# Kernel optimization log

Hardware: AMD Instinct MI355X
Metric: run time of the kernel (lower is better)

## Reference

```python
import jax, jax.numpy as jnp
import numpy as np

N_NODES = 100000


def gcn_conv(x, edge_index, W, b):
    """PyG-style GCNConv: h = D^-1/2 (A+I) D^-1/2 (x W) + b."""
    n = x.shape[0]
    loop = jnp.arange(n)
    src = jnp.concatenate([edge_index[0], loop])  # [E+N]
    dst = jnp.concatenate([edge_index[1], loop])  # [E+N]
    # degree computed on destination nodes (PyG gcn_norm with self-loops)
    deg = jnp.zeros((n,), x.dtype).at[dst].add(1.0)
    dinv = jnp.where(deg > 0, jax.lax.rsqrt(deg), 0.0)
    norm = dinv[src] * dinv[dst]  # [E+N]
    h = x @ W  # [n, out]
    msg = h[src] * norm[:, None]  # gather + scale
    out = jax.ops.segment_sum(msg, dst, num_segments=n)  # scatter-add
    return out + b


def setup_inputs() -> dict:
    key = jax.random.key(0)
    ks = jax.random.split(key, 8)
    F_in, H, C = 64, 64, 32
    x = jax.random.normal(ks[0], (N_NODES, F_in), dtype=jnp.float32)
    edge_index = jax.random.randint(ks[1], (2, 1200000), 0, N_NODES, dtype=jnp.int64)
    W1 = jax.random.normal(ks[2], (F_in, H), dtype=jnp.float32) / np.sqrt(F_in)
    b1 = jnp.zeros((H,), jnp.float32)
    W2 = jax.random.normal(ks[3], (H, H), dtype=jnp.float32) / np.sqrt(H)
    b2 = jnp.zeros((H,), jnp.float32)
    Wc = jax.random.normal(ks[4], (H, C), dtype=jnp.float32) / np.sqrt(H)
    bc = jnp.zeros((C,), jnp.float32)
    return {"x": x, "edge_index": edge_index, "W1": W1, "b1": b1,
            "W2": W2, "b2": b2, "Wc": Wc, "bc": bc}


def reference(x, edge_index, W1, b1, W2, b2, Wc, bc):
    h = jnp.tanh(gcn_conv(x, edge_index, W1, b1))
    h = jnp.tanh(gcn_conv(h, edge_index, W2, b2))
    out = h @ Wc + bc
    return (out, h)
```

## Files before the change

kernel.cpp:

```cpp
#include <hip/hip_runtime.h>
#include <hip/hip_bf16.h>
#include <stdint.h>

#define CB_SHIFT 11
#define CB_NODES 2048
#define CAP 28672
#define PT 4096

static __device__ inline uint16_t f2bf(float f) {
    union { float f; uint32_t u; } v; v.f = f;
    uint32_t r = v.u + 0x7FFFu + ((v.u >> 16) & 1u);
    return (uint16_t)(r >> 16);
}
static __device__ inline float bflo(uint32_t u) {
    union { uint32_t u; float f; } v; v.u = u << 16; return v.f;
}
static __device__ inline float bfhi(uint32_t u) {
    union { uint32_t u; float f; } v; v.u = u & 0xFFFF0000u; return v.f;
}
static __device__ inline float tanh_fast(float x) {
    x = fminf(fmaxf(x, -20.f), 20.f);
    float e = __expf(2.f * x);
    return fmaf(-2.f, __builtin_amdgcn_rcpf(e + 1.f), 1.f);
}

__global__ __launch_bounds__(256) void k_init(const uint32_t* __restrict__ e, int E,
                                              int* __restrict__ flag, int* __restrict__ gcur) {
    int t = threadIdx.x;
    if (t < 64) {
        gcur[t] = 0;
        int cnt = E < 1024 ? E : 1024;
        int nz = 0;
        for (int i = t; i < cnt; i += 64) nz |= (e[2 * i + 1] != 0u);
        int any = __any(nz);
        if (t == 0) *flag = any ? 0 : 1;
    }
}

__global__ __launch_bounds__(256) void k_part(const uint32_t* __restrict__ e, int E,
                                              const int* __restrict__ flag,
                                              int* __restrict__ gcur,
                                              uint32_t* __restrict__ parts) {
    __shared__ int sh_hist[64], sh_off[64], sh_base[64];
    __shared__ uint32_t sh_buf[PT];
    __shared__ uint16_t sh_bkt[PT];
    int t = threadIdx.x;
    int tile0 = blockIdx.x * PT;
    int is64 = *flag;
    if (t < 64) sh_hist[t] = 0;
    __syncthreads();

    uint32_t rec[16]; int cb[16], rank[16];
    const uint2* e2p = (const uint2*)e;
    for (int j = 0; j < 16; ++j) {
        int idx = tile0 + j * 256 + t;
        cb[j] = -1;
        if (idx < E) {
            uint32_t s, d;
            if (is64) { s = e2p[idx].x; d = e2p[E + idx].x; }
            else      { s = e[idx];     d = e[E + idx]; }
            rec[j] = (s << CB_SHIFT) | (d & (CB_NODES - 1));
            cb[j] = (int)(d >> CB_SHIFT);
            rank[j] = atomicAdd(&sh_hist[cb[j]], 1);
        }
    }
    __syncthreads();
    if (t < 64) {
        int cnt = sh_hist[t];
        int incl = cnt;
        for (int o = 1; o < 64; o <<= 1) {
            int v = __shfl_up(incl, o);
            if (t >= o) incl += v;
        }
        sh_off[t] = incl - cnt;
        sh_base[t] = (cnt > 0) ? atomicAdd(&gcur[t], cnt) : 0;
    }
    __syncthreads();
    for (int j = 0; j < 16; ++j) {
        if (cb[j] >= 0) {
            int slot = sh_off[cb[j]] + rank[j];
            sh_buf[slot] = rec[j];
            sh_bkt[slot] = (uint16_t)cb[j];
        }
    }
    __syncthreads();
    int total = min(PT, E - tile0);
    for (int i = t; i < total; i += 256) {
        int b = sh_bkt[i];
        int dest = sh_base[b] + (i - sh_off[b]);
        parts[(size_t)b * CAP + dest] = sh_buf[i];
    }
}

__global__ __launch_bounds__(1024) void k_build(const uint32_t* __restrict__ parts,
                                                const int* __restrict__ gcur,
                                                float* __restrict__ dinv,
                                                int* __restrict__ rowbeg,
                                                int* __restrict__ rowend,
                                                uint32_t* __restrict__ col, int N) {
    __shared__ int hist[CB_NODES], cur[CB_NODES], wsum[16];
    int t = threadIdx.x, cb = blockIdx.x;
    int lane = t & 63, w = t >> 6;
    for (int i = t; i < CB_NODES; i += 1024) hist[i] = 0;
    __syncthreads();
    int cnt = gcur[cb];
    const uint32_t* rp = parts + (size_t)cb * CAP;
    for (int i = t; i < cnt; i += 1024) atomicAdd(&hist[rp[i] & (CB_NODES - 1)], 1);
    __syncthreads();
    int h0 = hist[2 * t], h1 = hist[2 * t + 1];
    int s = h0 + h1;
    int incl = s;
    for (int o = 1; o < 64; o <<= 1) {
        int v = __shfl_up(incl, o);
        if (lane >= o) incl += v;
    }
    if (lane == 63) wsum[w] = incl;
    __syncthreads();
    if (t < 16) {
        int v = wsum[t];
        int inc2 = v;
        for (int o = 1; o < 16; o <<= 1) {
            int u = __shfl_up(inc2, o);
            if (t >= o) inc2 += u;
        }
        wsum[t] = inc2 - v;
    }
    __syncthreads();
    int ex = wsum[w] + incl - s;
    int b0 = ex, b1 = ex + h0;
    cur[2 * t] = b0;
    cur[2 * t + 1] = b1;
    int n0 = cb * CB_NODES;
    int base = cb * CAP;
    if (n0 + 2 * t < N) {
        rowbeg[n0 + 2 * t] = base + b0;
        rowend[n0 + 2 * t] = base + b0 + h0;
        dinv[n0 + 2 * t] = rsqrtf((float)(h0 + 1));
    }
    if (n0 + 2 * t + 1 < N) {
        rowbeg[n0 + 2 * t + 1] = base + b1;
        rowend[n0 + 2 * t + 1] = base + b1 + h1;
        dinv[n0 + 2 * t + 1] = rsqrtf((float)(h1 + 1));
    }
    __syncthreads();
    for (int i = t; i < cnt; i += 1024) {
        uint32_t rec = rp[i];
        int pos = atomicAdd(&cur[rec & (CB_NODES - 1)], 1);
        col[base + pos] = rec >> CB_SHIFT;
    }
}

__global__ __launch_bounds__(256) void k_gemm(const float* __restrict__ A,
                                              const float* __restrict__ W,
                                              const float* __restrict__ dinv,
                                              uint16_t* __restrict__ out, int N) {
    __shared__ __align__(16) float xT[64 * 68];
    __shared__ __align__(16) float Wl[64 * 64];
    int t = threadIdx.x;
#pragma unroll
    for (int j = 0; j < 16; ++j) Wl[j * 256 + t] = W[j * 256 + t];
    int n0 = blockIdx.x * 64;
    int nvalid = min(64, N - n0);
#pragma unroll
    for (int j = 0; j < 4; ++j) {
        int flat = j * 256 + t;
        int node = flat >> 4;
        int k4 = (flat & 15) * 4;
        float4 v = make_float4(0.f, 0.f, 0.f, 0.f);
        if (node < nvalid) v = *(const float4*)&A[(size_t)(n0 + node) * 64 + k4];
        xT[(k4 + 0) * 68 + node] = v.x;
        xT[(k4 + 1) * 68 + node] = v.y;
        xT[(k4 + 2) * 68 + node] = v.z;
        xT[(k4 + 3) * 68 + node] = v.w;
    }
    __syncthreads();
    int ng = t >> 4, cg = t & 15;
    float acc[4][4] = {};
#pragma unroll 8
    for (int k = 0; k < 64; ++k) {
        float4 a = *(const float4*)&xT[k * 68 + 4 * ng];
        float4 b = *(const float4*)&Wl[k * 64 + 4 * cg];
        float av[4] = {a.x, a.y, a.z, a.w};
        float bv[4] = {b.x, b.y, b.z, b.w};
#pragma unroll
        for (int i = 0; i < 4; ++i)
#pragma unroll
            for (int j = 0; j < 4; ++j) acc[i][j] = fmaf(av[i], bv[j], acc[i][j]);
    }
#pragma unroll
    for (int i = 0; i < 4; ++i) {
        int ln = 4 * ng + i;
        if (ln < nvalid) {
            int n = n0 + ln;
            float dv = dinv[n];
            ushort4 o;
            o.x = f2bf(acc[i][0] * dv);
            o.y = f2bf(acc[i][1] * dv);
            o.z = f2bf(acc[i][2] * dv);
            o.w = f2bf(acc[i][3] * dv);
            *(ushort4*)&out[(size_t)n * 64 + 4 * cg] = o;
        }
    }
}

__global__ __launch_bounds__(512) void k_agg(const uint16_t* __restrict__ h,
                                             const int* __restrict__ rowbeg,
                                             const int* __restrict__ rowend,
                                             const uint32_t* __restrict__ col,
                                             const float* __restrict__ dinv,
                                             const float* __restrict__ bias,
                                             const float* __restrict__ ,
                                             float* __restrict__ out, int N) {
    int t = threadIdx.x;
    int lane = t & 63, wid = t >> 6;
    int slot = lane >> 3;
    int g = lane & 7;
    const uint4* hp = (const uint4*)h;
    float bv[8];
#pragma unroll
    for (int j = 0; j < 8; ++j) bv[j] = bias[g * 8 + j];
    int n = (blockIdx.x * 8 + wid) * 8 + slot;
    int rs = 0, deg = 0;
    if (n < N) { rs = rowbeg[n]; deg = rowend[n] - rs; }
    int m = deg;
#pragma unroll
    for (int o = 1; o < 64; o <<= 1) m = max(m, __shfl_xor(m, o));
    float acc[8] = {};
#pragma unroll 2
    for (int it = 0; it < m; ++it) {
        if (it < deg) {
            int src = (int)col[rs + it];
            uint4 v = hp[(size_t)src * 8 + g];
            acc[0] += bflo(v.x); acc[1] += bfhi(v.x);
            acc[2] += bflo(v.y); acc[3] += bfhi(v.y);
            acc[4] += bflo(v.z); acc[5] += bfhi(v.z);
            acc[6] += bflo(v.w); acc[7] += bfhi(v.w);
        }
    }
    if (n < N) {
        float di = dinv[n];
        uint4 v = hp[(size_t)n * 8 + g];
        float hn[8] = {bflo(v.x), bfhi(v.x), bflo(v.y), bfhi(v.y),
                       bflo(v.z), bfhi(v.z), bflo(v.w), bfhi(v.w)};
        __align__(16) float o[8];
#pragma unroll
        for (int j = 0; j < 8; ++j)
            o[j] = tanh_fast(di * (acc[j] + hn[j]) + bv[j]);
        *(float4*)&out[(size_t)n * 64 + g * 8]     = *(float4*)&o[0];
        *(float4*)&out[(size_t)n * 64 + g * 8 + 4] = *(float4*)&o[4];
    }
}

__global__ __launch_bounds__(256) void k_cls(const float* __restrict__ A,
                                             const float* __restrict__ W,
                                             const float* __restrict__ bc,
                                             float* __restrict__ out, int N) {
    __shared__ __align__(16) float xT[64 * 68];
    __shared__ __align__(16) float Wl[64 * 32];
    int t = threadIdx.x;
#pragma unroll
    for (int j = 0; j < 8; ++j) Wl[j * 256 + t] = W[j * 256 + t];
    int n0 = blockIdx.x * 64;
    int nvalid = min(64, N - n0);
#pragma unroll
    for (int j = 0; j < 4; ++j) {
        int flat = j * 256 + t;
        int node = flat >> 4;
        int k4 = (flat & 15) * 4;
        float4 v = make_float4(0.f, 0.f, 0.f, 0.f);
        if (node < nvalid) v = *(const float4*)&A[(size_t)(n0 + node) * 64 + k4];
        xT[(k4 + 0) * 68 + node] = v.x;
        xT[(k4 + 1) * 68 + node] = v.y;
        xT[(k4 + 2) * 68 + node] = v.z;
        xT[(k4 + 3) * 68 + node] = v.w;
    }
    __syncthreads();
    int ng = t >> 4, cg = t & 15;
    float acc[4][2] = {};
#pragma unroll 8
    for (int k = 0; k < 64; ++k) {
        float4 a = *(const float4*)&xT[k * 68 + 4 * ng];
        float2 b = *(const float2*)&Wl[k * 32 + 2 * cg];
        float av[4] = {a.x, a.y, a.z, a.w};
#pragma unroll
        for (int i = 0; i < 4; ++i) {
            acc[i][0] = fmaf(av[i], b.x, acc[i][0]);
            acc[i][1] = fmaf(av[i], b.y, acc[i][1]);
        }
    }
    float2 bcv = *(const float2*)&bc[2 * cg];
#pragma unroll
    for (int i = 0; i < 4; ++i) {
        int ln = 4 * ng + i;
        if (ln < nvalid) {
            int n = n0 + ln;
            float2 o = make_float2(acc[i][0] + bcv.x, acc[i][1] + bcv.y);
            *(float2*)&out[(size_t)n * 32 + 2 * cg] = o;
        }
    }
}

extern "C" void kernel_launch(void* const* d_in, const int* in_sizes, int n_in,
                              void* d_out, int out_size, void* d_ws, size_t ws_size,
                              hipStream_t stream) {
    const float*    x     = (const float*)d_in[0];
    const uint32_t* edges = (const uint32_t*)d_in[1];
    const float*    W1    = (const float*)d_in[2];
    const float*    b1    = (const float*)d_in[3];
    const float*    W2    = (const float*)d_in[4];
    const float*    b2    = (const float*)d_in[5];
    const float*    Wc    = (const float*)d_in[6];
    const float*    bc    = (const float*)d_in[7];

    const int N   = in_sizes[0] / 64;
    const int E   = in_sizes[1] / 2;
    const int NBC = (N + CB_NODES - 1) >> CB_SHIFT;
    const int NTG = (N + 63) / 64;
    const int NTP = (E + PT - 1) / PT;
    const int NAG = (N + 63) / 64;

    char* w = (char*)d_ws;
    size_t off = 0;
    auto alloc = [&](size_t bytes) {
        void* p = w + off;
        off = (off + bytes + 255) & ~(size_t)255;
        return p;
    };
    int*      flag   = (int*)alloc(4);
    int*      gcur   = (int*)alloc(64 * 4);
    float*    dinv   = (float*)alloc((size_t)N * 4);
    uint32_t* parts  = (uint32_t*)alloc((size_t)NBC * CAP * 4);
    uint32_t* col    = (uint32_t*)alloc((size_t)NBC * CAP * 4);
    int*      rowbeg = (int*)alloc((size_t)N * 4);
    int*      rowend = (int*)alloc((size_t)N * 4);
    uint16_t* bufA   = (uint16_t*)alloc((size_t)N * 64 * 2);

    float* outc = (float*)d_out;
    float* hfin = outc + (size_t)N * 32;

    hipLaunchKernelGGL(k_init, dim3(1), dim3(256), 0, stream, edges, E, flag, gcur);
    hipLaunchKernelGGL(k_part, dim3(NTP), dim3(256), 0, stream, edges, E, flag, gcur, parts);
    hipLaunchKernelGGL(k_build, dim3(NBC), dim3(1024), 0, stream, parts, gcur, dinv, rowbeg, rowend, col, N);

    hipLaunchKernelGGL(k_gemm, dim3(NTG), dim3(256), 0, stream, x, W1, dinv, bufA, N);
    hipLaunchKernelGGL(k_agg, dim3(NAG), dim3(512), 0, stream, bufA, rowbeg, rowend, col, dinv, b1, (const float*)nullptr, hfin, N);
    hipLaunchKernelGGL(k_gemm, dim3(NTG), dim3(256), 0, stream, hfin, W2, dinv, bufA, N);
    hipLaunchKernelGGL(k_agg, dim3(NAG), dim3(512), 0, stream, bufA, rowbeg, rowend, col, dinv, b2, (const float*)nullptr, hfin, N);
    hipLaunchKernelGGL(k_cls, dim3(NTG), dim3(256), 0, stream, hfin, Wc, bc, outc, N);
}
```

Measured before the change: 257.1 us.

## Sort nodes by degree for aggregation to reduce wavefront divergence

Builds a global degree histogram during CSR construction, scans it, and writes a degree-sorted permutation of nodes packed as (row start, degree, node id, dinv). The aggregation kernel walks this permutation, so the 8 nodes sharing a wavefront have similar degrees and the loop bound set by the wavefront's maximum degree wastes fewer iterations. The unroll factor of the aggregation loop also goes from 2 to 4. The cost is two extra small kernels, an extra 16-byte-per-node array, and output writes that now land at scattered node rows instead of contiguous ones.

```diff
diff --git a/kernel.cpp b/kernel.cpp
--- a/kernel.cpp
+++ b/kernel.cpp
@@ -25,8 +25,10 @@
 }
 
 __global__ __launch_bounds__(256) void k_init(const uint32_t* __restrict__ e, int E,
-                                              int* __restrict__ flag, int* __restrict__ gcur) {
-    int t = threadIdx.x;
+                                              int* __restrict__ flag, int* __restrict__ gcur,
+                                              int* __restrict__ dhist) {
+    int t = threadIdx.x;
+    dhist[t] = 0;
     if (t < 64) {
         gcur[t] = 0;
         int cnt = E < 1024 ? E : 1024;
@@ -97,17 +99,22 @@
                                                 float* __restrict__ dinv,
                                                 int* __restrict__ rowbeg,
                                                 int* __restrict__ rowend,
-                                                uint32_t* __restrict__ col, int N) {
-    __shared__ int hist[CB_NODES], cur[CB_NODES], wsum[16];
+                                                uint32_t* __restrict__ col,
+                                                int* __restrict__ dhist, int N) {
+    __shared__ int hist[CB_NODES], cur[CB_NODES], wsum[16], dh[256];
     int t = threadIdx.x, cb = blockIdx.x;
     int lane = t & 63, w = t >> 6;
     for (int i = t; i < CB_NODES; i += 1024) hist[i] = 0;
+    if (t < 256) dh[t] = 0;
     __syncthreads();
     int cnt = gcur[cb];
     const uint32_t* rp = parts + (size_t)cb * CAP;
     for (int i = t; i < cnt; i += 1024) atomicAdd(&hist[rp[i] & (CB_NODES - 1)], 1);
     __syncthreads();
     int h0 = hist[2 * t], h1 = hist[2 * t + 1];
+    int n0 = cb * CB_NODES;
+    if (n0 + 2 * t < N)     atomicAdd(&dh[min(h0, 255)], 1);
+    if (n0 + 2 * t + 1 < N) atomicAdd(&dh[min(h1, 255)], 1);
     int s = h0 + h1;
     int incl = s;
     for (int o = 1; o < 64; o <<= 1) {
@@ -130,7 +137,6 @@
     int b0 = ex, b1 = ex + h0;
     cur[2 * t] = b0;
     cur[2 * t + 1] = b1;
-    int n0 = cb * CB_NODES;
     int base = cb * CAP;
     if (n0 + 2 * t < N) {
         rowbeg[n0 + 2 * t] = base + b0;
@@ -143,10 +149,52 @@
         dinv[n0 + 2 * t + 1] = rsqrtf((float)(h1 + 1));
     }
     __syncthreads();
+    if (t < 256 && dh[t]) atomicAdd(&dhist[t], dh[t]);
     for (int i = t; i < cnt; i += 1024) {
         uint32_t rec = rp[i];
         int pos = atomicAdd(&cur[rec & (CB_NODES - 1)], 1);
         col[base + pos] = rec >> CB_SHIFT;
+    }
+}
+
+__global__ __launch_bounds__(256) void k_dscan(const int* __restrict__ dhist,
+                                               int* __restrict__ dcur) {
+    __shared__ int sd[256];
+    int t = threadIdx.x;
+    int v = dhist[t];
+    sd[t] = v; __syncthreads();
+    for (int o = 1; o < 256; o <<= 1) {
+        int x = (t >= o) ? sd[t - o] : 0;
+        __syncthreads();
+        sd[t] += x;
+        __syncthreads();
+    }
+    dcur[t] = sd[t] - v;
+}
+
+__global__ __launch_bounds__(1024) void k_dperm(const int* __restrict__ rowbeg,
+                                                const int* __restrict__ rowend,
+                                                const float* __restrict__ dinv,
+                                                int* __restrict__ dcur,
+                                                int4* __restrict__ perm4, int N) {
+    __shared__ int lh[256], lbase[256];
+    int t = threadIdx.x;
+    if (t < 256) lh[t] = 0;
+    __syncthreads();
+    int n = blockIdx.x * 1024 + t;
+    int c = 0, rank = 0, beg = 0, deg = 0;
+    if (n < N) {
+        beg = rowbeg[n];
+        deg = rowend[n] - beg;
+        c = min(deg, 255);
+        rank = atomicAdd(&lh[c], 1);
+    }
+    __syncthreads();
+    if (t < 256 && lh[t]) lbase[t] = atomicAdd(&dcur[t], lh[t]);
+    __syncthreads();
+    if (n < N) {
+        int pos = lbase[c] + rank;
+        perm4[pos] = make_int4(beg, deg, n, __float_as_int(dinv[n]));
     }
 }
 
@@ -204,12 +252,9 @@
 }
 
 __global__ __launch_bounds__(512) void k_agg(const uint16_t* __restrict__ h,
-                                             const int* __restrict__ rowbeg,
-                                             const int* __restrict__ rowend,
+                                             const int4* __restrict__ perm4,
                                              const uint32_t* __restrict__ col,
-                                             const float* __restrict__ dinv,
                                              const float* __restrict__ bias,
-                                             const float* __restrict__ ,
                                              float* __restrict__ out, int N) {
     int t = threadIdx.x;
     int lane = t & 63, wid = t >> 6;
@@ -219,14 +264,17 @@
     float bv[8];
 #pragma unroll
     for (int j = 0; j < 8; ++j) bv[j] = bias[g * 8 + j];
-    int n = (blockIdx.x * 8 + wid) * 8 + slot;
-    int rs = 0, deg = 0;
-    if (n < N) { rs = rowbeg[n]; deg = rowend[n] - rs; }
+    int idx = (blockIdx.x * 8 + wid) * 8 + slot;
+    bool valid = idx < N;
+    int4 pi = make_int4(0, 0, 0, 0);
+    if (valid) pi = perm4[idx];
+    int rs = pi.x, deg = valid ? pi.y : 0, n = pi.z;
+    float di = __int_as_float(pi.w);
     int m = deg;
 #pragma unroll
     for (int o = 1; o < 64; o <<= 1) m = max(m, __shfl_xor(m, o));
     float acc[8] = {};
-#pragma unroll 2
+#pragma unroll 4
     for (int it = 0; it < m; ++it) {
         if (it < deg) {
             int src = (int)col[rs + it];
@@ -237,8 +285,7 @@
             acc[6] += bflo(v.w); acc[7] += bfhi(v.w);
         }
     }
-    if (n < N) {
-        float di = dinv[n];
+    if (valid) {
         uint4 v = hp[(size_t)n * 8 + g];
         float hn[8] = {bflo(v.x), bfhi(v.x), bflo(v.y), bfhi(v.y),
                        bflo(v.z), bfhi(v.z), bflo(v.w), bfhi(v.w)};
@@ -318,6 +365,7 @@
     const int NTG = (N + 63) / 64;
     const int NTP = (E + PT - 1) / PT;
     const int NAG = (N + 63) / 64;
+    const int NDP = (N + 1023) / 1024;
 
     char* w = (char*)d_ws;
     size_t off = 0;
@@ -328,23 +376,28 @@
     };
     int*      flag   = (int*)alloc(4);
     int*      gcur   = (int*)alloc(64 * 4);
+    int*      dhist  = (int*)alloc(256 * 4);
+    int*      dcur   = (int*)alloc(256 * 4);
     float*    dinv   = (float*)alloc((size_t)N * 4);
     uint32_t* parts  = (uint32_t*)alloc((size_t)NBC * CAP * 4);
     uint32_t* col    = (uint32_t*)alloc((size_t)NBC * CAP * 4);
     int*      rowbeg = (int*)alloc((size_t)N * 4);
     int*      rowend = (int*)alloc((size_t)N * 4);
+    int4*     perm4  = (int4*)alloc((size_t)N * 16);
     uint16_t* bufA   = (uint16_t*)alloc((size_t)N * 64 * 2);
 
     float* outc = (float*)d_out;
     float* hfin = outc + (size_t)N * 32;
 
-    hipLaunchKernelGGL(k_init, dim3(1), dim3(256), 0, stream, edges, E, flag, gcur);
+    hipLaunchKernelGGL(k_init, dim3(1), dim3(256), 0, stream, edges, E, flag, gcur, dhist);
     hipLaunchKernelGGL(k_part, dim3(NTP), dim3(256), 0, stream, edges, E, flag, gcur, parts);
-    hipLaunchKernelGGL(k_build, dim3(NBC), dim3(1024), 0, stream, parts, gcur, dinv, rowbeg, rowend, col, N);
+    hipLaunchKernelGGL(k_build, dim3(NBC), dim3(1024), 0, stream, parts, gcur, dinv, rowbeg, rowend, col, dhist, N);
+    hipLaunchKernelGGL(k_dscan, dim3(1), dim3(256), 0, stream, dhist, dcur);
+    hipLaunchKernelGGL(k_dperm, dim3(NDP), dim3(1024), 0, stream, rowbeg, rowend, dinv, dcur, perm4, N);
 
     hipLaunchKernelGGL(k_gemm, dim3(NTG), dim3(256), 0, stream, x, W1, dinv, bufA, N);
-    hipLaunchKernelGGL(k_agg, dim3(NAG), dim3(512), 0, stream, bufA, rowbeg, rowend, col, dinv, b1, (const float*)nullptr, hfin, N);
+    hipLaunchKernelGGL(k_agg, dim3(NAG), dim3(512), 0, stream, bufA, perm4, col, b1, hfin, N);
     hipLaunchKernelGGL(k_gemm, dim3(NTG), dim3(256), 0, stream, hfin, W2, dinv, bufA, N);
-    hipLaunchKernelGGL(k_agg, dim3(NAG), dim3(512), 0, stream, bufA, rowbeg, rowend, col, dinv, b2, (const float*)nullptr, hfin, N);
+    hipLaunchKernelGGL(k_agg, dim3(NAG), dim3(512), 0, stream, bufA, perm4, col, b2, hfin, N);
     hipLaunchKernelGGL(k_cls, dim3(NTG), dim3(256), 0, stream, hfin, Wc, bc, outc, N);
 }
```

Result: no change. 260.6 us (+1.3%).
